# Kernel tuning notes

Hardware: AMD Instinct MI355X
Metric: run time of the kernel (lower is better)

## Reference

```python
import jax, jax.numpy as jnp
import numpy as np

N_USERS, N_ITEMS, EMB_DIM, N_INTENTS, N_EDGES, N_LAYERS = 50000, 100000, 64, 128, 3000000, 2
N_NODES = N_USERS + N_ITEMS


def _l2norm(x, eps=1e-8):
    # F.normalize(p=2, dim=-1, eps): x / max(||x||, eps)
    n = jnp.sqrt(jnp.sum(x * x, axis=-1, keepdims=True))
    return x / jnp.maximum(n, eps)


def setup_inputs() -> dict:
    key = jax.random.key(0)
    k0, k1, k2, k3, k4, k5 = jax.random.split(key, 6)
    xav_e = np.sqrt(2.0 / (N_NODES + EMB_DIM)).astype(np.float32)
    xav_i = np.sqrt(2.0 / (EMB_DIM + N_INTENTS)).astype(np.float32)
    return {
        "user_emb": jax.random.normal(k0, (N_USERS, EMB_DIM), jnp.float32) * xav_e,
        "item_emb": jax.random.normal(k1, (N_ITEMS, EMB_DIM), jnp.float32) * xav_e,
        "user_intent": jax.random.normal(k2, (EMB_DIM, N_INTENTS), jnp.float32) * xav_i,
        "item_intent": jax.random.normal(k3, (EMB_DIM, N_INTENTS), jnp.float32) * xav_i,
        "all_h": jax.random.randint(k4, (N_EDGES,), 0, N_NODES, jnp.int32),
        "all_t": jax.random.randint(k5, (N_EDGES,), 0, N_NODES, jnp.int32),
    }


def reference(user_emb, item_emb, user_intent, item_intent, all_h, all_t):
    E = all_h.shape[0]

    def spmm(vals, x):
        # y[h] += vals * x[t]  over edges  (torch_sparse.spmm)
        return jax.ops.segment_sum(vals[:, None] * x[all_t], all_h, num_segments=N_NODES)

    # _cal_sparse_adj: G = D^-1/2 A D^-1/2 on the unweighted edge list
    deg = jax.ops.segment_sum(jnp.ones((E,), jnp.float32), all_h, num_segments=N_NODES)
    d_inv_sqrt = jnp.where(deg > 0, deg, 1.0) ** -0.5 * (deg > 0)
    g_values = d_inv_sqrt[all_h] * d_inv_sqrt[all_t]

    def adaptive_values(src):
        # _adaptive_mask: cosine-sim edge weights, row-normalized
        he = _l2norm(src[all_h])
        te = _l2norm(src[all_t])
        edge_alpha = (jnp.sum(he * te, axis=1) + 1.0) * 0.5  # in [0,1]
        row_sum = jax.ops.segment_sum(edge_alpha, all_h, num_segments=N_NODES)
        d_inv = jnp.where(row_sum > 0, 1.0 / jnp.where(row_sum > 0, row_sum, 1.0), 0.0)
        return d_inv[all_h] * edge_alpha

    emb = jnp.concatenate([user_emb, item_emb], axis=0)  # [N, d]
    acc = emb
    for _ in range(N_LAYERS):
        gnn = spmm(g_values, emb)
        u, it = emb[:N_USERS], emb[N_USERS:]
        u_int = jax.nn.softmax(u @ user_intent, axis=1) @ user_intent.T
        i_int = jax.nn.softmax(it @ item_intent, axis=1) @ item_intent.T
        int_e = jnp.concatenate([u_int, i_int], axis=0)
        gaa = spmm(adaptive_values(gnn), emb)
        iaa = spmm(adaptive_values(int_e), emb)
        emb = gnn + int_e + gaa + iaa + emb
        acc = acc + emb
    # torch: sum over stacked layer embeddings == initial + each layer output
    return acc
```

## Files before the change

kernel.cpp:

```cpp
#include <hip/hip_runtime.h>
#include <hip/hip_bf16.h>

#define N_USERS   50000
#define N_ITEMS   100000
#define N_NODES   150000
#define DIM       64
#define N_INTENTS 128
#define N_EDGES   3000000
#define PSHIFT    9
#define PROWS     (1 << PSHIFT)
#define NPART     ((N_NODES + PROWS - 1) >> PSHIFT)
#define CHUNK     16384
#define NCHB      ((N_EDGES + CHUNK - 1) / CHUNK)

typedef __attribute__((ext_vector_type(8))) short short8v;
typedef __attribute__((ext_vector_type(4))) float f32x4;
typedef __attribute__((ext_vector_type(2))) float f32x2;

template<int CTRL>
static __device__ __forceinline__ float dpp_ror_add(float x){
  int t = __builtin_amdgcn_update_dpp(0, __builtin_bit_cast(int, x),
                                      CTRL, 0xF, 0xF, true);
  return x + __builtin_bit_cast(float, t);
}
static __device__ __forceinline__ float row16_allsum(float x){
  x = dpp_ror_add<0x128>(x);
  x = dpp_ror_add<0x124>(x);
  x = dpp_ror_add<0x122>(x);
  x = dpp_ror_add<0x121>(x);
  return x;
}
template<int CTRL>
static __device__ __forceinline__ float dpp_ror_max(float x){
  int t = __builtin_amdgcn_update_dpp(0, __builtin_bit_cast(int, x),
                                      CTRL, 0xF, 0xF, true);
  return fmaxf(x, __builtin_bit_cast(float, t));
}
static __device__ __forceinline__ float row16_allmax(float x){
  x = dpp_ror_max<0x128>(x);
  x = dpp_ror_max<0x124>(x);
  x = dpp_ror_max<0x122>(x);
  x = dpp_ror_max<0x121>(x);
  return x;
}

static __device__ __forceinline__ unsigned short f2bf(float x){
  __hip_bfloat16 h = __float2bfloat16(x);
  return __builtin_bit_cast(unsigned short, h);
}
static __device__ __forceinline__ float bf_lo(unsigned int v){
  return __builtin_bit_cast(float, v << 16);
}
static __device__ __forceinline__ float bf_hi(unsigned int v){
  return __builtin_bit_cast(float, v & 0xFFFF0000u);
}
static __device__ __forceinline__ float bfval(unsigned short h){
  return __builtin_bit_cast(float, (unsigned int)h << 16);
}
static __device__ __forceinline__ void split2(float x, unsigned short& hi,
                                              unsigned short& lo){
  hi = f2bf(x);
  lo = f2bf(x - bfval(hi));
}

static __device__ __forceinline__ void fp8dec8(uint2 v, float* f){
  f32x2 a = __builtin_amdgcn_cvt_pk_f32_fp8(v.x, false);
  f32x2 b = __builtin_amdgcn_cvt_pk_f32_fp8(v.x, true);
  f32x2 c = __builtin_amdgcn_cvt_pk_f32_fp8(v.y, false);
  f32x2 d = __builtin_amdgcn_cvt_pk_f32_fp8(v.y, true);
  f[0]=a[0]; f[1]=a[1]; f[2]=b[0]; f[3]=b[1];
  f[4]=c[0]; f[5]=c[1]; f[6]=d[0]; f[7]=d[1];
}
static __device__ __forceinline__ unsigned char f2fp8(float x){
  return (unsigned char)(__builtin_amdgcn_cvt_pk_fp8_f32(x, x, 0, false) & 0xFF);
}

__global__ void k_init(const float* __restrict__ ue, const float* __restrict__ ie,
                       float* __restrict__ emb, float* __restrict__ acc,
                       unsigned short* __restrict__ embb){
  int i = blockIdx.x * 256 + threadIdx.x;
  if (i >= N_NODES * DIM) return;
  float v = (i < N_USERS * DIM) ? ue[i] : ie[i - N_USERS * DIM];
  emb[i] = v; acc[i] = v; embb[i] = f2bf(v);
}

__global__ void k_embd0(const float* __restrict__ emb, const float* __restrict__ dis,
                        uint2* __restrict__ embd2){
  int i = blockIdx.x * 256 + threadIdx.x;
  if (i >= N_NODES * 16) return;
  float d = dis[i >> 4];
  float4 v = ((const float4*)emb)[i];
  uint2 ob;
  ob.x = (unsigned)f2bf(d * v.x) | ((unsigned)f2bf(d * v.y) << 16);
  ob.y = (unsigned)f2bf(d * v.z) | ((unsigned)f2bf(d * v.w) << 16);
  embd2[i] = ob;
}

__global__ void k_deg(const int* __restrict__ h, int* __restrict__ deg){
  int e = blockIdx.x * 256 + threadIdx.x;
  if (e < N_EDGES) atomicAdd(&deg[h[e]], 1);
}

__global__ void k_scan1(const int* __restrict__ deg, int* __restrict__ tmp,
                        int* __restrict__ aux){
  __shared__ int s[256];
  int t = threadIdx.x, i = blockIdx.x * 256 + t;
  int v = (i < N_NODES) ? deg[i] : 0;
  s[t] = v; __syncthreads();
  for (int off = 1; off < 256; off <<= 1){
    int x = (t >= off) ? s[t - off] : 0;
    __syncthreads();
    s[t] += x;
    __syncthreads();
  }
  if (i < N_NODES) tmp[i] = s[t];
  if (t == 255) aux[blockIdx.x] = s[255];
}

__global__ __launch_bounds__(1024) void k_scan2(int* __restrict__ aux, int n){
  __shared__ int s[1024];
  int t = threadIdx.x;
  int v = (t < n) ? aux[t] : 0;
  s[t] = v; __syncthreads();
  for (int off = 1; off < 1024; off <<= 1){
    int x = (t >= off) ? s[t - off] : 0;
    __syncthreads();
    s[t] += x;
    __syncthreads();
  }
  if (t < n) aux[t] = s[t] - v;
}

__global__ void k_rowptr(const int* __restrict__ tmp, const int* __restrict__ deg,
                         const int* __restrict__ aux, int* __restrict__ rp,
                         float* __restrict__ dis, int* __restrict__ gcur){
  int i = blockIdx.x * 256 + threadIdx.x;
  if (i < N_NODES){
    int v = aux[i >> 8] + tmp[i] - deg[i];
    rp[i] = v;
    int d = deg[i];
    dis[i] = (d > 0) ? (1.f / sqrtf((float)d)) : 0.f;
    if ((i & (PROWS - 1)) == 0) gcur[i >> PSHIFT] = v;
  }
  if (i == 0) rp[N_NODES] = N_EDGES;
}

__global__ __launch_bounds__(256) void k_part1(const int* __restrict__ h,
                                               const int* __restrict__ t,
                                               int* __restrict__ gcur,
                                               unsigned int* __restrict__ stg){
  __shared__ int hist[NPART];
  __shared__ int base[NPART];
  __shared__ int cnt2[NPART];
  int tid = threadIdx.x;
  int s = blockIdx.x * CHUNK;
  int e = min(s + CHUNK, N_EDGES);
  for (int p = tid; p < NPART; p += 256){ hist[p] = 0; cnt2[p] = 0; }
  __syncthreads();
  for (int i = s + tid; i < e; i += 256)
    atomicAdd(&hist[h[i] >> PSHIFT], 1);
  __syncthreads();
  for (int p = tid; p < NPART; p += 256){
    int c = hist[p];
    base[p] = c ? atomicAdd(&gcur[p], c) : 0;
  }
  __syncthreads();
  for (int i = s + tid; i < e; i += 256){
    int hh = h[i];
    int part = hh >> PSHIFT;
    int pos = base[part] + atomicAdd(&cnt2[part], 1);
    stg[pos] = ((unsigned)t[i] << PSHIFT) | (unsigned)(hh & (PROWS - 1));
  }
}

__global__ __launch_bounds__(256) void k_part2(const int* __restrict__ rp,
                                               const unsigned int* __restrict__ stg,
                                               int* __restrict__ t_csr){
  __shared__ int cur[PROWS];
  int b = blockIdx.x, tid = threadIdx.x;
  int row0 = b << PSHIFT;
  int rows = min(PROWS, N_NODES - row0);
  for (int i = tid; i < rows; i += 256) cur[i] = rp[row0 + i];
  __syncthreads();
  int s = rp[row0], e = rp[row0 + rows];
  for (int i = s + tid; i < e; i += 256){
    unsigned int v = stg[i];
    int pos = atomicAdd(&cur[v & (PROWS - 1)], 1);
    t_csr[pos] = (int)(v >> PSHIFT);
  }
}

__global__ void k_spmm_gnn(const int* __restrict__ rp, const int* __restrict__ t_csr,
                           const float* __restrict__ dis,
                           const unsigned short* __restrict__ embd,
                           float* __restrict__ gnn, unsigned char* __restrict__ hg8){
  int w = (blockIdx.x * 256 + threadIdx.x) >> 6;
  int lane = threadIdx.x & 63;
  if (w >= N_NODES) return;
  int slot = lane >> 3, sub = lane & 7;
  int s = rp[w], e = rp[w + 1];
  float a0=0.f,a1=0.f,a2=0.f,a3=0.f,a4=0.f,a5=0.f,a6=0.f,a7=0.f;
  for (int i = s + slot; i < e; i += 8){
    int t = t_csr[i];
    uint4 ev = *(const uint4*)(embd + (size_t)t * 64 + 8 * sub);
    a0 += bf_lo(ev.x); a1 += bf_hi(ev.x);
    a2 += bf_lo(ev.y); a3 += bf_hi(ev.y);
    a4 += bf_lo(ev.z); a5 += bf_hi(ev.z);
    a6 += bf_lo(ev.w); a7 += bf_hi(ev.w);
  }
#pragma unroll
  for (int m = 8; m <= 32; m <<= 1){
    a0 += __shfl_xor(a0, m, 64); a1 += __shfl_xor(a1, m, 64);
    a2 += __shfl_xor(a2, m, 64); a3 += __shfl_xor(a3, m, 64);
    a4 += __shfl_xor(a4, m, 64); a5 += __shfl_xor(a5, m, 64);
    a6 += __shfl_xor(a6, m, 64); a7 += __shfl_xor(a7, m, 64);
  }
  float dw = dis[w];
  float g0 = dw*a0, g1 = dw*a1, g2 = dw*a2, g3 = dw*a3;
  float g4 = dw*a4, g5 = dw*a5, g6 = dw*a6, g7 = dw*a7;
  float sq = g0*g0 + g1*g1 + g2*g2 + g3*g3 + g4*g4 + g5*g5 + g6*g6 + g7*g7;
#pragma unroll
  for (int m = 1; m <= 4; m <<= 1) sq += __shfl_xor(sq, m, 64);
  float invn = 1.f / fmaxf(sqrtf(sq), 1e-8f);
  if (slot == 0){
    float4 v0 = make_float4(g0, g1, g2, g3);
    float4 v1 = make_float4(g4, g5, g6, g7);
    ((float4*)gnn)[w * 16 + 2 * sub]     = v0;
    ((float4*)gnn)[w * 16 + 2 * sub + 1] = v1;
    unsigned int d0 = __builtin_amdgcn_cvt_pk_fp8_f32(g0*invn, g1*invn, 0, false);
    d0 = __builtin_amdgcn_cvt_pk_fp8_f32(g2*invn, g3*invn, d0, true);
    unsigned int d1 = __builtin_amdgcn_cvt_pk_fp8_f32(g4*invn, g5*invn, 0, false);
    d1 = __builtin_amdgcn_cvt_pk_fp8_f32(g6*invn, g7*invn, d1, true);
    uint2 o; o.x = d0; o.y = d1;
    *(uint2*)(hg8 + (size_t)w * 128 + 8 * sub) = o;
  }
}

__global__ void k_wprep(const float* __restrict__ wu, const float* __restrict__ wi,
                        unsigned short* __restrict__ wbuf){
  const float* W = blockIdx.x ? wi : wu;
  unsigned short* seg = wbuf + blockIdx.x * 32768;
  int tid = threadIdx.x;
  for (int i = tid; i < DIM * N_INTENTS; i += 256){
    unsigned short h, l; split2(W[i], h, l);
    seg[16384 + i] = h; seg[24576 + i] = l;
  }
  for (int idx = tid; idx < 16 * 64; idx += 256){
    int f = idx >> 6, lane = idx & 63;
    int nt = f >> 1, ks = f & 1, g = lane >> 4, c = lane & 15;
    int in = 16 * nt + c;
#pragma unroll
    for (int e = 0; e < 8; e++){
      int d = 8 * g + e + 32 * ks;
      unsigned short h, l; split2(W[d * N_INTENTS + in], h, l);
      seg[f * 512 + lane * 8 + e] = h;
      seg[8192 + f * 512 + lane * 8 + e] = l;
    }
  }
}

__global__ __launch_bounds__(256) void k_intent_mfma(
    const unsigned short* __restrict__ wseg, const float* __restrict__ emb,
    unsigned short* __restrict__ out_bf, unsigned char* __restrict__ hg8,
    int base_node, int count){
  __shared__ __align__(16) unsigned int Pl[4][2048];
  int wid = threadIdx.x >> 6, lane = threadIdx.x & 63;
  int tile = blockIdx.x * 4 + wid;
  if (tile * 16 >= count) return;
  int g = lane >> 4, c = lane & 15;

  const float4* erow = (const float4*)(emb + (size_t)(base_node + tile * 16 + c) * DIM);
  float4 ea0 = erow[2 * g],     eb0 = erow[2 * g + 1];
  float4 ea1 = erow[8 + 2 * g], eb1 = erow[9 + 2 * g];
  short8v ehi[2], elo[2];
  {
    float xs[16] = {ea0.x, ea0.y, ea0.z, ea0.w, eb0.x, eb0.y, eb0.z, eb0.w,
                    ea1.x, ea1.y, ea1.z, ea1.w, eb1.x, eb1.y, eb1.z, eb1.w};
#pragma unroll
    for (int ksi = 0; ksi < 2; ksi++)
#pragma unroll
      for (int e = 0; e < 8; e++){
        unsigned short h, l; split2(xs[ksi * 8 + e], h, l);
        ehi[ksi][e] = (short)h; elo[ksi][e] = (short)l;
      }
  }

  const uint4* w1hi = (const uint4*)wseg;
  const uint4* w1lo = (const uint4*)(wseg + 8192);
  f32x4 acc1[8];
#pragma unroll
  for (int nt = 0; nt < 8; nt++){
    f32x4 a = {0.f, 0.f, 0.f, 0.f};
#pragma unroll
    for (int ks = 0; ks < 2; ks++){
      short8v wh = __builtin_bit_cast(short8v, w1hi[(nt * 2 + ks) * 64 + lane]);
      short8v wl = __builtin_bit_cast(short8v, w1lo[(nt * 2 + ks) * 64 + lane]);
      a = __builtin_amdgcn_mfma_f32_16x16x32_bf16(ehi[ks], wh, a, 0, 0, 0);
      a = __builtin_amdgcn_mfma_f32_16x16x32_bf16(elo[ks], wh, a, 0, 0, 0);
      a = __builtin_amdgcn_mfma_f32_16x16x32_bf16(ehi[ks], wl, a, 0, 0, 0);
    }
    acc1[nt] = a;
  }

  unsigned int* pw = &Pl[wid][0];
#pragma unroll
  for (int r = 0; r < 4; r++){
    float m = acc1[0][r];
#pragma unroll
    for (int nt = 1; nt < 8; nt++) m = fmaxf(m, acc1[nt][r]);
    m = row16_allmax(m);
    float p[8];
    float s = 0.f;
#pragma unroll
    for (int nt = 0; nt < 8; nt++){ p[nt] = __expf(acc1[nt][r] - m); s += p[nt]; }
    s = row16_allsum(s);
    float inv = 1.f / s;
    int node = 4 * g + r;
    int swz = (node & 7) << 2;
    int base = node * 128 + c;
#pragma unroll
    for (int nt = 0; nt < 8; nt++){
      float v = p[nt] * inv;
      unsigned short h, l; split2(v, h, l);
      pw[(base + 16 * nt) ^ swz] = (unsigned int)h | ((unsigned int)l << 16);
    }
  }

  const uint4* pr = (const uint4*)pw;
  short8v phf[4], plf[4];
  int sw = (c & 7) << 2;
#pragma unroll
  for (int ks = 0; ks < 4; ks++){
    int i0 = c * 128 + 8 * g + 32 * ks;
    uint4 ra = pr[(i0 ^ sw) >> 2];
    uint4 rb = pr[((i0 + 4) ^ sw) >> 2];
    unsigned int q[8] = {ra.x, ra.y, ra.z, ra.w, rb.x, rb.y, rb.z, rb.w};
#pragma unroll
    for (int e = 0; e < 8; e++){
      phf[ks][e] = (short)(q[e] & 0xFFFFu);
      plf[ks][e] = (short)(q[e] >> 16);
    }
  }

  const uint4* w2hi = (const uint4*)(wseg + 16384);
  const uint4* w2lo = (const uint4*)(wseg + 24576);
  f32x4 acc2[4];
#pragma unroll
  for (int nt = 0; nt < 4; nt++){
    f32x4 a = {0.f, 0.f, 0.f, 0.f};
#pragma unroll
    for (int ks = 0; ks < 4; ks++){
      int fi = (16 * nt + c) * 16 + ks * 4 + g;
      short8v wh = __builtin_bit_cast(short8v, w2hi[fi]);
      short8v wl = __builtin_bit_cast(short8v, w2lo[fi]);
      a = __builtin_amdgcn_mfma_f32_16x16x32_bf16(phf[ks], wh, a, 0, 0, 0);
      a = __builtin_amdgcn_mfma_f32_16x16x32_bf16(plf[ks], wh, a, 0, 0, 0);
      a = __builtin_amdgcn_mfma_f32_16x16x32_bf16(phf[ks], wl, a, 0, 0, 0);
    }
    acc2[nt] = a;
  }

#pragma unroll
  for (int r = 0; r < 4; r++){
    float sq = 0.f;
#pragma unroll
    for (int nt = 0; nt < 4; nt++) sq = fmaf(acc2[nt][r], acc2[nt][r], sq);
    sq = row16_allsum(sq);
    float invn = 1.f / fmaxf(sqrtf(sq), 1e-8f);
    size_t node = (size_t)(base_node + tile * 16 + 4 * g + r);
    unsigned char* hw = hg8 + node * 128 + 64;
    size_t obase = node * DIM + c;
#pragma unroll
    for (int nt = 0; nt < 4; nt++){
      float v = acc2[nt][r];
      out_bf[obase + 16 * nt] = f2bf(v);
      hw[16 * nt + c] = f2fp8(v * invn);
    }
  }
}

__global__ void k_adafuse(const int* __restrict__ rp, const int* __restrict__ t_csr,
                          const unsigned char* __restrict__ hg8,
                          const uint2* __restrict__ inte_bf2,
                          const uint2* __restrict__ embb2,
                          const float* __restrict__ emb,
                          const float* __restrict__ dis,
                          float* __restrict__ gnn_io, float* __restrict__ acc,
                          uint2* __restrict__ embb_next2,
                          uint2* __restrict__ embd_next2){
  int w = (blockIdx.x * 256 + threadIdx.x) >> 6;
  int lane = threadIdx.x & 63;
  if (w >= N_NODES) return;
  int slot = lane >> 4, sub = lane & 15;
  const uint2* hg2 = (const uint2*)hg8;
  float wv[8];
  fp8dec8(hg2[(size_t)w * 16 + sub], wv);
  bool isA = sub < 8;
  int s = rp[w], e = rp[w + 1];
  float4 s1 = make_float4(0.f, 0.f, 0.f, 0.f);
  float4 s2 = make_float4(0.f, 0.f, 0.f, 0.f);
  float r1 = 0.f, r2 = 0.f;
  for (int i = s + slot; i < e; i += 4){
    int t = t_csr[i];
    float tv[8];
    fp8dec8(hg2[(size_t)t * 16 + sub], tv);
    float part = wv[0]*tv[0] + wv[1]*tv[1] + wv[2]*tv[2] + wv[3]*tv[3]
               + wv[4]*tv[4] + wv[5]*tv[5] + wv[6]*tv[6] + wv[7]*tv[7];
    part += __shfl_xor(part, 1, 64);
    part += __shfl_xor(part, 2, 64);
    part += __shfl_xor(part, 4, 64);
    float other = __shfl_xor(part, 8, 64);
    float p = isA ? part : other;
    float q = isA ? other : part;
    float a1 = fmaf(p, 0.5f, 0.5f);
    float a2 = fmaf(q, 0.5f, 0.5f);
    r1 += a1; r2 += a2;
    uint2 ev = embb2[(size_t)t * 16 + sub];
    float v0 = bf_lo(ev.x), v1 = bf_hi(ev.x), v2 = bf_lo(ev.y), v3 = bf_hi(ev.y);
    s1.x = fmaf(a1, v0, s1.x); s1.y = fmaf(a1, v1, s1.y);
    s1.z = fmaf(a1, v2, s1.z); s1.w = fmaf(a1, v3, s1.w);
    s2.x = fmaf(a2, v0, s2.x); s2.y = fmaf(a2, v1, s2.y);
    s2.z = fmaf(a2, v2, s2.z); s2.w = fmaf(a2, v3, s2.w);
  }
#pragma unroll
  for (int m = 16; m <= 32; m <<= 1){
    s1.x += __shfl_xor(s1.x, m, 64); s1.y += __shfl_xor(s1.y, m, 64);
    s1.z += __shfl_xor(s1.z, m, 64); s1.w += __shfl_xor(s1.w, m, 64);
    s2.x += __shfl_xor(s2.x, m, 64); s2.y += __shfl_xor(s2.y, m, 64);
    s2.z += __shfl_xor(s2.z, m, 64); s2.w += __shfl_xor(s2.w, m, 64);
    r1   += __shfl_xor(r1,   m, 64); r2   += __shfl_xor(r2,   m, 64);
  }
  float d1 = (r1 > 0.f) ? 1.f / r1 : 0.f;
  float d2 = (r2 > 0.f) ? 1.f / r2 : 0.f;
  if (slot == 0){
    int idx4 = w * 16 + sub;
    float4 gg = ((float4*)gnn_io)[idx4];
    uint2 it = inte_bf2[idx4];
    float4 em = ((const float4*)emb)[idx4];
    float4 nv;
    nv.x = gg.x + bf_lo(it.x) + em.x + d1 * s1.x + d2 * s2.x;
    nv.y = gg.y + bf_hi(it.x) + em.y + d1 * s1.y + d2 * s2.y;
    nv.z = gg.z + bf_lo(it.y) + em.z + d1 * s1.z + d2 * s2.z;
    nv.w = gg.w + bf_hi(it.y) + em.w + d1 * s1.w + d2 * s2.w;
    ((float4*)gnn_io)[idx4] = nv;
    float4 ac = ((float4*)acc)[idx4];
    ac.x += nv.x; ac.y += nv.y; ac.z += nv.z; ac.w += nv.w;
    ((float4*)acc)[idx4] = ac;
    uint2 ob;
    ob.x = (unsigned)f2bf(nv.x) | ((unsigned)f2bf(nv.y) << 16);
    ob.y = (unsigned)f2bf(nv.z) | ((unsigned)f2bf(nv.w) << 16);
    embb_next2[idx4] = ob;
    float dw = dis[w];
    uint2 od;
    od.x = (unsigned)f2bf(dw * nv.x) | ((unsigned)f2bf(dw * nv.y) << 16);
    od.y = (unsigned)f2bf(dw * nv.z) | ((unsigned)f2bf(dw * nv.w) << 16);
    embd_next2[idx4] = od;
  }
}

extern "C" void kernel_launch(void* const* d_in, const int* in_sizes, int n_in,
                              void* d_out, int out_size, void* d_ws, size_t ws_size,
                              hipStream_t stream){
  const float* ue = (const float*)d_in[0];
  const float* ie = (const float*)d_in[1];
  const float* wu = (const float*)d_in[2];
  const float* wi = (const float*)d_in[3];
  const int* all_h = (const int*)d_in[4];
  const int* all_t = (const int*)d_in[5];
  float* acc = (float*)d_out;

  char* p = (char*)d_ws;
  auto take = [&](size_t bytes)->char*{
    char* r = p; p += (bytes + 255) & ~size_t(255); return r;
  };
  float*  embA  = (float*)take(sizeof(float) * N_NODES * DIM);
  float*  embB  = (float*)take(sizeof(float) * N_NODES * DIM);
  unsigned char* hg8 = (unsigned char*)take((size_t)N_NODES * 128);
  unsigned short* inte_bf = (unsigned short*)take(sizeof(short) * N_NODES * DIM);
  unsigned short* embbA   = (unsigned short*)take(sizeof(short) * N_NODES * DIM);
  unsigned short* embbB   = (unsigned short*)take(sizeof(short) * N_NODES * DIM);
  unsigned short* embd    = (unsigned short*)take(sizeof(short) * N_NODES * DIM);
  unsigned short* wbuf    = (unsigned short*)take(sizeof(short) * 2 * 32768);
  int*    t_csr = (int*)take(sizeof(int) * N_EDGES);
  float*  dis   = (float*)take(sizeof(float) * N_NODES);
  int*    deg   = (int*)take(sizeof(int) * N_NODES);
  int*    tmp   = (int*)take(sizeof(int) * N_NODES);
  int*    aux   = (int*)take(sizeof(int) * 1024);
  int*    rp    = (int*)take(sizeof(int) * (N_NODES + 1));
  int*    gcur  = (int*)take(sizeof(int) * NPART);
  if ((size_t)(p - (char*)d_ws) > ws_size) return;
  unsigned int* stg = (unsigned int*)hg8;

  const int ELEM_B  = (N_NODES * DIM + 255) / 256;
  const int ELEM4_B = (N_NODES * 16 + 255) / 256;
  const int NODEW_B = (N_NODES * 64 + 255) / 256;
  const int EDGE_B  = (N_EDGES + 255) / 256;
  const int NODE_B  = (N_NODES + 255) / 256;

  hipMemsetAsync(deg, 0, sizeof(int) * N_NODES, stream);
  k_init<<<ELEM_B, 256, 0, stream>>>(ue, ie, embA, acc, embbA);
  k_wprep<<<2, 256, 0, stream>>>(wu, wi, wbuf);
  k_deg<<<EDGE_B, 256, 0, stream>>>(all_h, deg);
  k_scan1<<<NODE_B, 256, 0, stream>>>(deg, tmp, aux);
  k_scan2<<<1, 1024, 0, stream>>>(aux, NODE_B);
  k_rowptr<<<NODE_B, 256, 0, stream>>>(tmp, deg, aux, rp, dis, gcur);
  k_embd0<<<ELEM4_B, 256, 0, stream>>>(embA, dis, (uint2*)embd);
  k_part1<<<NCHB, 256, 0, stream>>>(all_h, all_t, gcur, stg);
  k_part2<<<NPART, 256, 0, stream>>>(rp, stg, t_csr);

  const int UT_B = ((N_USERS / 16) + 3) / 4;
  const int IT_B = ((N_ITEMS / 16) + 3) / 4;

  float* eA = embA;
  float* eB = embB;
  unsigned short* ebA = embbA;
  unsigned short* ebB = embbB;
  for (int layer = 0; layer < 2; layer++){
    k_spmm_gnn<<<NODEW_B, 256, 0, stream>>>(rp, t_csr, dis, embd, eB, hg8);
    k_intent_mfma<<<UT_B, 256, 0, stream>>>(wbuf, eA, inte_bf, hg8, 0, N_USERS);
    k_intent_mfma<<<IT_B, 256, 0, stream>>>(wbuf + 32768, eA, inte_bf, hg8,
                                            N_USERS, N_ITEMS);
    k_adafuse<<<NODEW_B, 256, 0, stream>>>(rp, t_csr, hg8,
                                           (const uint2*)inte_bf,
                                           (const uint2*)ebA,
                                           eA, dis, eB, acc,
                                           (uint2*)ebB, (uint2*)embd);
    float* t = eA; eA = eB; eB = t;
    unsigned short* tb = ebA; ebA = ebB; ebB = tb;
  }
}
```

Before: 948.9 us.

## Interleave fp8 direction vectors and bf16 embeddings into per-node 256-byte records

Packs the two fp8 normalized direction vectors (64B each) and the bf16 embedding (128B) for each node into a single 256-byte record. The edge gather in the adaptive-aggregation kernel then touches one contiguous region per neighbour instead of two separate arrays. It also merges the user and item intent launches into one grid and skips writing next-layer buffers on the last layer. The cost is double-buffered record storage and more complex indexing.

```diff
diff --git a/kernel.cpp b/kernel.cpp
--- a/kernel.cpp
+++ b/kernel.cpp
@@ -12,6 +12,11 @@
 #define NPART     ((N_NODES + PROWS - 1) >> PSHIFT)
 #define CHUNK     16384
 #define NCHB      ((N_EDGES + CHUNK - 1) / CHUNK)
+#define RECB      256
+
+#define UT_TILES  (N_USERS / 16)
+#define TOT_TILES ((N_USERS + N_ITEMS) / 16)
+#define INT_B     ((TOT_TILES + 3) / 4)
 
 typedef __attribute__((ext_vector_type(8))) short short8v;
 typedef __attribute__((ext_vector_type(4))) float f32x4;
@@ -71,29 +76,38 @@
   f[0]=a[0]; f[1]=a[1]; f[2]=b[0]; f[3]=b[1];
   f[4]=c[0]; f[5]=c[1]; f[6]=d[0]; f[7]=d[1];
 }
+static __device__ __forceinline__ unsigned int fp8pack4(float a, float b,
+                                                        float c, float d){
+  unsigned int v = __builtin_amdgcn_cvt_pk_fp8_f32(a, b, 0, false);
+  return __builtin_amdgcn_cvt_pk_fp8_f32(c, d, v, true);
+}
 static __device__ __forceinline__ unsigned char f2fp8(float x){
   return (unsigned char)(__builtin_amdgcn_cvt_pk_fp8_f32(x, x, 0, false) & 0xFF);
 }
 
 __global__ void k_init(const float* __restrict__ ue, const float* __restrict__ ie,
-                       float* __restrict__ emb, float* __restrict__ acc,
-                       unsigned short* __restrict__ embb){
+                       float* __restrict__ emb, float* __restrict__ acc){
   int i = blockIdx.x * 256 + threadIdx.x;
   if (i >= N_NODES * DIM) return;
   float v = (i < N_USERS * DIM) ? ue[i] : ie[i - N_USERS * DIM];
-  emb[i] = v; acc[i] = v; embb[i] = f2bf(v);
+  emb[i] = v; acc[i] = v;
 }
 
 __global__ void k_embd0(const float* __restrict__ emb, const float* __restrict__ dis,
-                        uint2* __restrict__ embd2){
+                        uint2* __restrict__ embd2, unsigned char* __restrict__ rec0){
   int i = blockIdx.x * 256 + threadIdx.x;
   if (i >= N_NODES * 16) return;
-  float d = dis[i >> 4];
+  int n = i >> 4, sub = i & 15;
+  float d = dis[n];
   float4 v = ((const float4*)emb)[i];
   uint2 ob;
   ob.x = (unsigned)f2bf(d * v.x) | ((unsigned)f2bf(d * v.y) << 16);
   ob.y = (unsigned)f2bf(d * v.z) | ((unsigned)f2bf(d * v.w) << 16);
   embd2[i] = ob;
+  uint2 eb;
+  eb.x = (unsigned)f2bf(v.x) | ((unsigned)f2bf(v.y) << 16);
+  eb.y = (unsigned)f2bf(v.z) | ((unsigned)f2bf(v.w) << 16);
+  *(uint2*)(rec0 + (size_t)n * RECB + 128 + 8 * sub) = eb;
 }
 
 __global__ void k_deg(const int* __restrict__ h, int* __restrict__ deg){
@@ -193,7 +207,7 @@
 __global__ void k_spmm_gnn(const int* __restrict__ rp, const int* __restrict__ t_csr,
                            const float* __restrict__ dis,
                            const unsigned short* __restrict__ embd,
-                           float* __restrict__ gnn, unsigned char* __restrict__ hg8){
+                           float* __restrict__ gnn, unsigned char* __restrict__ rec){
   int w = (blockIdx.x * 256 + threadIdx.x) >> 6;
   int lane = threadIdx.x & 63;
   if (w >= N_NODES) return;
@@ -227,12 +241,10 @@
     float4 v1 = make_float4(g4, g5, g6, g7);
     ((float4*)gnn)[w * 16 + 2 * sub]     = v0;
     ((float4*)gnn)[w * 16 + 2 * sub + 1] = v1;
-    unsigned int d0 = __builtin_amdgcn_cvt_pk_fp8_f32(g0*invn, g1*invn, 0, false);
-    d0 = __builtin_amdgcn_cvt_pk_fp8_f32(g2*invn, g3*invn, d0, true);
-    unsigned int d1 = __builtin_amdgcn_cvt_pk_fp8_f32(g4*invn, g5*invn, 0, false);
-    d1 = __builtin_amdgcn_cvt_pk_fp8_f32(g6*invn, g7*invn, d1, true);
-    uint2 o; o.x = d0; o.y = d1;
-    *(uint2*)(hg8 + (size_t)w * 128 + 8 * sub) = o;
+    uint2 o;
+    o.x = fp8pack4(g0*invn, g1*invn, g2*invn, g3*invn);
+    o.y = fp8pack4(g4*invn, g5*invn, g6*invn, g7*invn);
+    *(uint2*)(rec + (size_t)w * RECB + 8 * sub) = o;
   }
 }
 
@@ -260,16 +272,18 @@
 }
 
 __global__ __launch_bounds__(256) void k_intent_mfma(
-    const unsigned short* __restrict__ wseg, const float* __restrict__ emb,
-    unsigned short* __restrict__ out_bf, unsigned char* __restrict__ hg8,
-    int base_node, int count){
+    const unsigned short* __restrict__ wbuf, const float* __restrict__ emb,
+    unsigned short* __restrict__ out_bf, unsigned char* __restrict__ rec){
   __shared__ __align__(16) unsigned int Pl[4][2048];
   int wid = threadIdx.x >> 6, lane = threadIdx.x & 63;
   int tile = blockIdx.x * 4 + wid;
-  if (tile * 16 >= count) return;
+  if (tile >= TOT_TILES) return;
+  int node0; const unsigned short* wseg;
+  if (tile < UT_TILES){ node0 = tile * 16;                         wseg = wbuf; }
+  else                { node0 = N_USERS + (tile - UT_TILES) * 16;  wseg = wbuf + 32768; }
   int g = lane >> 4, c = lane & 15;
 
-  const float4* erow = (const float4*)(emb + (size_t)(base_node + tile * 16 + c) * DIM);
+  const float4* erow = (const float4*)(emb + (size_t)(node0 + c) * DIM);
   float4 ea0 = erow[2 * g],     eb0 = erow[2 * g + 1];
   float4 ea1 = erow[8 + 2 * g], eb1 = erow[9 + 2 * g];
   short8v ehi[2], elo[2];
@@ -367,8 +381,8 @@
     for (int nt = 0; nt < 4; nt++) sq = fmaf(acc2[nt][r], acc2[nt][r], sq);
     sq = row16_allsum(sq);
     float invn = 1.f / fmaxf(sqrtf(sq), 1e-8f);
-    size_t node = (size_t)(base_node + tile * 16 + 4 * g + r);
-    unsigned char* hw = hg8 + node * 128 + 64;
+    size_t node = (size_t)(node0 + 4 * g + r);
+    unsigned char* hw = rec + node * RECB + 64;
     size_t obase = node * DIM + c;
 #pragma unroll
     for (int nt = 0; nt < 4; nt++){
@@ -380,21 +394,21 @@
 }
 
 __global__ void k_adafuse(const int* __restrict__ rp, const int* __restrict__ t_csr,
-                          const unsigned char* __restrict__ hg8,
+                          const unsigned char* __restrict__ rec,
                           const uint2* __restrict__ inte_bf2,
-                          const uint2* __restrict__ embb2,
                           const float* __restrict__ emb,
                           const float* __restrict__ dis,
                           float* __restrict__ gnn_io, float* __restrict__ acc,
-                          uint2* __restrict__ embb_next2,
-                          uint2* __restrict__ embd_next2){
+                          uint2* __restrict__ embd_next2,
+                          unsigned char* __restrict__ rec_next,
+                          int write_next){
   int w = (blockIdx.x * 256 + threadIdx.x) >> 6;
   int lane = threadIdx.x & 63;
   if (w >= N_NODES) return;
   int slot = lane >> 4, sub = lane & 15;
-  const uint2* hg2 = (const uint2*)hg8;
+  const unsigned char* wrec = rec + (size_t)w * RECB;
   float wv[8];
-  fp8dec8(hg2[(size_t)w * 16 + sub], wv);
+  fp8dec8(*(const uint2*)(wrec + 8 * sub), wv);
   bool isA = sub < 8;
   int s = rp[w], e = rp[w + 1];
   float4 s1 = make_float4(0.f, 0.f, 0.f, 0.f);
@@ -402,8 +416,9 @@
   float r1 = 0.f, r2 = 0.f;
   for (int i = s + slot; i < e; i += 4){
     int t = t_csr[i];
+    const unsigned char* tr = rec + (size_t)t * RECB;
     float tv[8];
-    fp8dec8(hg2[(size_t)t * 16 + sub], tv);
+    fp8dec8(*(const uint2*)(tr + 8 * sub), tv);
     float part = wv[0]*tv[0] + wv[1]*tv[1] + wv[2]*tv[2] + wv[3]*tv[3]
                + wv[4]*tv[4] + wv[5]*tv[5] + wv[6]*tv[6] + wv[7]*tv[7];
     part += __shfl_xor(part, 1, 64);
@@ -415,7 +430,7 @@
     float a1 = fmaf(p, 0.5f, 0.5f);
     float a2 = fmaf(q, 0.5f, 0.5f);
     r1 += a1; r2 += a2;
-    uint2 ev = embb2[(size_t)t * 16 + sub];
+    uint2 ev = *(const uint2*)(tr + 128 + 8 * sub);
     float v0 = bf_lo(ev.x), v1 = bf_hi(ev.x), v2 = bf_lo(ev.y), v3 = bf_hi(ev.y);
     s1.x = fmaf(a1, v0, s1.x); s1.y = fmaf(a1, v1, s1.y);
     s1.z = fmaf(a1, v2, s1.z); s1.w = fmaf(a1, v3, s1.w);
@@ -446,15 +461,17 @@
     float4 ac = ((float4*)acc)[idx4];
     ac.x += nv.x; ac.y += nv.y; ac.z += nv.z; ac.w += nv.w;
     ((float4*)acc)[idx4] = ac;
-    uint2 ob;
-    ob.x = (unsigned)f2bf(nv.x) | ((unsigned)f2bf(nv.y) << 16);
-    ob.y = (unsigned)f2bf(nv.z) | ((unsigned)f2bf(nv.w) << 16);
-    embb_next2[idx4] = ob;
-    float dw = dis[w];
-    uint2 od;
-    od.x = (unsigned)f2bf(dw * nv.x) | ((unsigned)f2bf(dw * nv.y) << 16);
-    od.y = (unsigned)f2bf(dw * nv.z) | ((unsigned)f2bf(dw * nv.w) << 16);
-    embd_next2[idx4] = od;
+    if (write_next){
+      float dw = dis[w];
+      uint2 od;
+      od.x = (unsigned)f2bf(dw * nv.x) | ((unsigned)f2bf(dw * nv.y) << 16);
+      od.y = (unsigned)f2bf(dw * nv.z) | ((unsigned)f2bf(dw * nv.w) << 16);
+      embd_next2[idx4] = od;
+      uint2 ob;
+      ob.x = (unsigned)f2bf(nv.x) | ((unsigned)f2bf(nv.y) << 16);
+      ob.y = (unsigned)f2bf(nv.z) | ((unsigned)f2bf(nv.w) << 16);
+      *(uint2*)(rec_next + (size_t)w * RECB + 128 + 8 * sub) = ob;
+    }
   }
 }
 
@@ -475,10 +492,9 @@
   };
   float*  embA  = (float*)take(sizeof(float) * N_NODES * DIM);
   float*  embB  = (float*)take(sizeof(float) * N_NODES * DIM);
-  unsigned char* hg8 = (unsigned char*)take((size_t)N_NODES * 128);
+  unsigned char* rec0 = (unsigned char*)take((size_t)N_NODES * RECB);
+  unsigned char* rec1 = (unsigned char*)take((size_t)N_NODES * RECB);
   unsigned short* inte_bf = (unsigned short*)take(sizeof(short) * N_NODES * DIM);
-  unsigned short* embbA   = (unsigned short*)take(sizeof(short) * N_NODES * DIM);
-  unsigned short* embbB   = (unsigned short*)take(sizeof(short) * N_NODES * DIM);
   unsigned short* embd    = (unsigned short*)take(sizeof(short) * N_NODES * DIM);
   unsigned short* wbuf    = (unsigned short*)take(sizeof(short) * 2 * 32768);
   int*    t_csr = (int*)take(sizeof(int) * N_EDGES);
@@ -489,7 +505,7 @@
   int*    rp    = (int*)take(sizeof(int) * (N_NODES + 1));
   int*    gcur  = (int*)take(sizeof(int) * NPART);
   if ((size_t)(p - (char*)d_ws) > ws_size) return;
-  unsigned int* stg = (unsigned int*)hg8;
+  unsigned int* stg = (unsigned int*)rec1;
 
   const int ELEM_B  = (N_NODES * DIM + 255) / 256;
   const int ELEM4_B = (N_NODES * 16 + 255) / 256;
@@ -498,34 +514,29 @@
   const int NODE_B  = (N_NODES + 255) / 256;
 
   hipMemsetAsync(deg, 0, sizeof(int) * N_NODES, stream);
-  k_init<<<ELEM_B, 256, 0, stream>>>(ue, ie, embA, acc, embbA);
+  k_init<<<ELEM_B, 256, 0, stream>>>(ue, ie, embA, acc);
   k_wprep<<<2, 256, 0, stream>>>(wu, wi, wbuf);
   k_deg<<<EDGE_B, 256, 0, stream>>>(all_h, deg);
   k_scan1<<<NODE_B, 256, 0, stream>>>(deg, tmp, aux);
   k_scan2<<<1, 1024, 0, stream>>>(aux, NODE_B);
   k_rowptr<<<NODE_B, 256, 0, stream>>>(tmp, deg, aux, rp, dis, gcur);
-  k_embd0<<<ELEM4_B, 256, 0, stream>>>(embA, dis, (uint2*)embd);
+  k_embd0<<<ELEM4_B, 256, 0, stream>>>(embA, dis, (uint2*)embd, rec0);
   k_part1<<<NCHB, 256, 0, stream>>>(all_h, all_t, gcur, stg);
   k_part2<<<NPART, 256, 0, stream>>>(rp, stg, t_csr);
 
-  const int UT_B = ((N_USERS / 16) + 3) / 4;
-  const int IT_B = ((N_ITEMS / 16) + 3) / 4;
-
   float* eA = embA;
   float* eB = embB;
-  unsigned short* ebA = embbA;
-  unsigned short* ebB = embbB;
+  unsigned char* recC = rec0;
+  unsigned char* recN = rec1;
   for (int layer = 0; layer < 2; layer++){
-    k_spmm_gnn<<<NODEW_B, 256, 0, stream>>>(rp, t_csr, dis, embd, eB, hg8);
-    k_intent_mfma<<<UT_B, 256, 0, stream>>>(wbuf, eA, inte_bf, hg8, 0, N_USERS);
-    k_intent_mfma<<<IT_B, 256, 0, stream>>>(wbuf + 32768, eA, inte_bf, hg8,
-                                            N_USERS, N_ITEMS);
-    k_adafuse<<<NODEW_B, 256, 0, stream>>>(rp, t_csr, hg8,
+    k_spmm_gnn<<<NODEW_B, 256, 0, stream>>>(rp, t_csr, dis, embd, eB, recC);
+    k_intent_mfma<<<INT_B, 256, 0, stream>>>(wbuf, eA, inte_bf, recC);
+    k_adafuse<<<NODEW_B, 256, 0, stream>>>(rp, t_csr, recC,
                                            (const uint2*)inte_bf,
-                                           (const uint2*)ebA,
                                            eA, dis, eB, acc,
-                                           (uint2*)ebB, (uint2*)embd);
+                                           (uint2*)embd, recN,
+                                           layer == 0 ? 1 : 0);
     float* t = eA; eA = eB; eB = t;
-    unsigned short* tb = ebA; ebA = ebB; ebB = tb;
-  }
-}
+    unsigned char* tr = recC; recC = recN; recN = tr;
+  }
+}
```

New measurement: 937.9 us. No clear change (-1.2%).
